# Kernel optimization log

Hardware: AMD Instinct MI355X
Metric: run time of the kernel (lower is better)

The kernel has to match this reference:

```python
import jax, jax.numpy as jnp
import numpy as np

D_MODEL = 64

def setup_inputs() -> dict:
    key = jax.random.key(0)
    kq, kk, kv = jax.random.split(key, 3)
    B, S, D = 8, 4096, D_MODEL
    q = jax.random.normal(kq, (B, S, D), dtype=jnp.float32)
    k = jax.random.normal(kk, (B, S, D), dtype=jnp.float32)
    v = jax.random.normal(kv, (B, S, D), dtype=jnp.float32)
    return {"q": q, "k": k, "v": v}

def reference(q, k, v):
    # scores: [B, S, S], scaled by 1/sqrt(d_model)
    scale = 1.0 / jnp.sqrt(jnp.asarray(D_MODEL, dtype=jnp.float32))
    scores = jnp.einsum("bqd,bkd->bqk", q, k) * scale
    attn = jax.nn.softmax(scores, axis=-1)
    return jnp.einsum("bqk,bkd->bqd", attn, v)
```

## Files before the change

kernel.cpp:

```cpp
#include <hip/hip_runtime.h>
#include <hip/hip_bf16.h>

#define NB 8
#define NS 4096
#define ND 64
#define NROW (NB * NS)
#define NTILE (NS / 64)

typedef short v4s __attribute__((ext_vector_type(4)));
typedef short v8s __attribute__((ext_vector_type(8)));
typedef float v4f __attribute__((ext_vector_type(4)));

static __device__ __forceinline__ v4s pk4(float a, float b, float c, float d) {
    union { __hip_bfloat162 h[2]; v4s v; } u;
    float2 p0; p0.x = a; p0.y = b;
    float2 p1; p1.x = c; p1.y = d;
    u.h[0] = __float22bfloat162_rn(p0);
    u.h[1] = __float22bfloat162_rn(p1);
    return u.v;
}
static __device__ __forceinline__ v8s pk8(v4f x0, v4f x1) {
    union { v4s q[2]; v8s v; } u;
    u.q[0] = pk4(x0[0], x0[1], x0[2], x0[3]);
    u.q[1] = pk4(x1[0], x1[1], x1[2], x1[3]);
    return u.v;
}
static __device__ __forceinline__ float b2f(short s) {
    return __uint_as_float(((unsigned)(unsigned short)s) << 16);
}

__device__ __forceinline__ void gl16(const void* g, void* s) {
    __builtin_amdgcn_global_load_lds(
        (const __attribute__((address_space(1))) void*)g,
        (__attribute__((address_space(3))) void*)s, 16, 0, 0);
}

__global__ __launch_bounds__(256) void prep_frag(const float* __restrict__ K,
        const float* __restrict__ V, short* __restrict__ Kf,
        short* __restrict__ Vf) {
    __shared__ short TK[64][72];
    __shared__ short TV[64][72];
    const int bt = blockIdx.x;
    const int b  = bt >> 6;
    const int s0 = (bt & 63) * 64;
    const int i  = threadIdx.x;
    #pragma unroll
    for (int it = 0; it < 4; ++it) {
        int n2 = it * 256 + i;
        int r = n2 >> 4, c4 = (n2 & 15) * 4;
        const size_t src = ((size_t)b * NS + s0 + r) * ND + c4;
        v4f xk = *(const v4f*)(K + src);
        v4f xv = *(const v4f*)(V + src);
        *(v4s*)&TK[r][c4] = pk4(xk[0], xk[1], xk[2], xk[3]);
        *(v4s*)&TV[r][c4] = pk4(xv[0], xv[1], xv[2], xv[3]);
    }
    __syncthreads();
    const size_t ob = (size_t)bt * 4096;
    #pragma unroll
    for (int it = 0; it < 2; ++it) {
        int gi = it * 256 + i;
        int lane = gi & 63, h = lane >> 4, lc = lane & 15;
        {
            int g = gi >> 7, c = (gi >> 6) & 1;
            v8s kk = *(const v8s*)&TK[16 * g + lc][32 * c + 8 * h];
            *(v8s*)&Kf[ob + (size_t)gi * 8] = kk;
        }
        {
            int c2 = gi >> 8, g = (gi >> 6) & 3;
            v8s vv;
            #pragma unroll
            for (int j = 0; j < 4; ++j) {
                vv[j]     = TV[32 * c2 + 4 * h + j][16 * g + lc];
                vv[4 + j] = TV[32 * c2 + 16 + 4 * h + j][16 * g + lc];
            }
            *(v8s*)&Vf[ob + (size_t)gi * 8] = vv;
        }
    }
}

template <int SPLIT>
__global__ __launch_bounds__(256, 4) void fa_main(
        const float* __restrict__ Q, const short* __restrict__ Kf,
        const short* __restrict__ Vf, float* __restrict__ O,
        short* __restrict__ Opart, float2* __restrict__ stats) {
    __shared__ short Ksh[2][4096];
    __shared__ short Vsh[2][4096];

    const int t    = threadIdx.x;
    const int lane = t & 63;
    const int w    = t >> 6;
    const int lc   = lane & 15;
    const int h    = lane >> 4;

    const int bid  = blockIdx.x;
    const int b    = bid & 7;
    const int rest = bid >> 3;
    const int sp   = rest % SPLIT;
    const int qblk = rest / SPLIT;
    const int q0   = qblk * 128 + w * 32;

    const int TPS = NTILE / SPLIT;
    const int kt0 = sp * TPS;

    const float SCL = 0.125f * 1.4426950408889634f;

    v8s qf[2][2];
    #pragma unroll
    for (int u = 0; u < 2; ++u) {
        const float* qrow = Q + ((size_t)b * NS + q0 + 16 * u + lc) * ND + 8 * h;
        #pragma unroll
        for (int c = 0; c < 2; ++c) {
            v4f x0 = *(const v4f*)(qrow + 32 * c);
            v4f x1 = *(const v4f*)(qrow + 32 * c + 4);
            qf[u][c] = pk8(x0 * SCL, x1 * SCL);
        }
    }

    v4f o[2][4];
    #pragma unroll
    for (int u = 0; u < 2; ++u)
        #pragma unroll
        for (int g = 0; g < 4; ++g) o[u][g] = (v4f){0.f, 0.f, 0.f, 0.f};
    float lsum[2] = {0.f, 0.f};

    const short* kfb = Kf + ((size_t)(b * NTILE + kt0)) * 4096 + t * 8;
    const short* vfb = Vf + ((size_t)(b * NTILE + kt0)) * 4096 + t * 8;
    auto stage = [&](int i, int buf) {
        const short* kb = kfb + (size_t)i * 4096;
        const short* vb = vfb + (size_t)i * 4096;
        short* kd = &Ksh[buf][t * 8];
        short* vd = &Vsh[buf][t * 8];
        gl16(kb,        kd);
        gl16(kb + 2048, kd + 2048);
        gl16(vb,        vd);
        gl16(vb + 2048, vd + 2048);
    };

    auto body = [&](int cur) {
        const short* kp = &Ksh[cur][lane * 8];
        const short* vp = &Vsh[cur][lane * 8];

        v4f a[2][4];
        #pragma unroll
        for (int g = 0; g < 4; ++g) {
            a[0][g] = (v4f){0.f, 0.f, 0.f, 0.f};
            a[1][g] = (v4f){0.f, 0.f, 0.f, 0.f};
            #pragma unroll
            for (int c = 0; c < 2; ++c) {
                v8s ka = *(const v8s*)(kp + (g * 2 + c) * 512);
                a[0][g] = __builtin_amdgcn_mfma_f32_16x16x32_bf16(ka, qf[0][c], a[0][g], 0, 0, 0);
                a[1][g] = __builtin_amdgcn_mfma_f32_16x16x32_bf16(ka, qf[1][c], a[1][g], 0, 0, 0);
            }
        }

        union PB { v4s q[2]; v8s v; } pb[2][2];
        #pragma unroll
        for (int u = 0; u < 2; ++u) {
            float rs = 0.f;
            #pragma unroll
            for (int g = 0; g < 4; ++g) {
                float e0 = __builtin_amdgcn_exp2f(a[u][g][0]);
                float e1 = __builtin_amdgcn_exp2f(a[u][g][1]);
                float e2 = __builtin_amdgcn_exp2f(a[u][g][2]);
                float e3 = __builtin_amdgcn_exp2f(a[u][g][3]);
                rs += (e0 + e1) + (e2 + e3);
                pb[u][g >> 1].q[g & 1] = pk4(e0, e1, e2, e3);
            }
            lsum[u] += rs;
        }

        #pragma unroll
        for (int c2 = 0; c2 < 2; ++c2) {
            #pragma unroll
            for (int g = 0; g < 4; ++g) {
                v8s va = *(const v8s*)(vp + (c2 * 4 + g) * 512);
                o[0][g] = __builtin_amdgcn_mfma_f32_16x16x32_bf16(va, pb[0][c2].v, o[0][g], 0, 0, 0);
                o[1][g] = __builtin_amdgcn_mfma_f32_16x16x32_bf16(va, pb[1][c2].v, o[1][g], 0, 0, 0);
            }
        }
    };

    stage(0, 0);
    int cur = 0;
    for (int i = 0; i < TPS; ++i) {
        __syncthreads();
        if (i + 1 < TPS) stage(i + 1, cur ^ 1);
        body(cur);
        cur ^= 1;
    }

    #pragma unroll
    for (int u = 0; u < 2; ++u) {
        float ls = lsum[u];
        ls += __shfl_xor(ls, 16);
        ls += __shfl_xor(ls, 32);
        const float inv = 1.0f / ls;
        const int q = q0 + 16 * u + lc;
        if constexpr (SPLIT == 1) {
            float* orow = O + ((size_t)b * NS + q) * ND;
            #pragma unroll
            for (int g = 0; g < 4; ++g) {
                v4f rr = o[u][g] * inv;
                *(v4f*)(orow + 16 * g + 4 * h) = rr;
            }
        } else {
            short* op = Opart + ((size_t)sp * NROW + (size_t)b * NS + q) * ND;
            #pragma unroll
            for (int g = 0; g < 4; ++g) {
                v4f rr = o[u][g] * inv;
                *(v4s*)(op + 16 * g + 4 * h) = pk4(rr[0], rr[1], rr[2], rr[3]);
            }
            if (h == 0) {
                float2 st; st.x = 0.f; st.y = ls;
                stats[(size_t)sp * NROW + (size_t)b * NS + q] = st;
            }
        }
    }
}

template <int SPLIT>
__global__ __launch_bounds__(256) void fa_combine(const short* __restrict__ Opart,
        const float2* __restrict__ stats, float* __restrict__ O) {
    const int idx = blockIdx.x * 256 + threadIdx.x;
    const int row = idx >> 3;
    const int d8  = (idx & 7) * 8;
    float2 st[SPLIT];
    float M = -INFINITY;
    #pragma unroll
    for (int s = 0; s < SPLIT; ++s) {
        st[s] = stats[(size_t)s * NROW + row];
        M = fmaxf(M, st[s].x);
    }
    float wt[SPLIT], wsum = 0.f;
    #pragma unroll
    for (int s = 0; s < SPLIT; ++s) {
        wt[s] = exp2f(st[s].x - M) * st[s].y;
        wsum += wt[s];
    }
    float acc[8] = {0.f, 0.f, 0.f, 0.f, 0.f, 0.f, 0.f, 0.f};
    #pragma unroll
    for (int s = 0; s < SPLIT; ++s) {
        v8s x = *(const v8s*)&Opart[((size_t)s * NROW + row) * ND + d8];
        #pragma unroll
        for (int j = 0; j < 8; ++j) acc[j] += wt[s] * b2f(x[j]);
    }
    const float inv = 1.0f / wsum;
    v4f r0, r1;
    #pragma unroll
    for (int j = 0; j < 4; ++j) { r0[j] = acc[j] * inv; r1[j] = acc[4 + j] * inv; }
    *(v4f*)&O[(size_t)row * ND + d8]     = r0;
    *(v4f*)&O[(size_t)row * ND + d8 + 4] = r1;
}

__global__ __launch_bounds__(256) void fa_fallback(
        const float* __restrict__ Q, const float* __restrict__ K,
        const float* __restrict__ V, float* __restrict__ O) {
    __shared__ short Ksh[64][72];
    __shared__ short Vsh[64][72];
    const int t = threadIdx.x;
    const int lane = t & 63;
    const int w = t >> 6;
    const int lc = lane & 15;
    const int h  = lane >> 4;
    const int b  = blockIdx.x & 7;
    const int q0 = (blockIdx.x >> 3) * 128 + w * 32;
    const float SCL = 0.125f * 1.4426950408889634f;
    v8s qf[2][2];
    #pragma unroll
    for (int u = 0; u < 2; ++u) {
        const float* qrow = Q + ((size_t)b * NS + q0 + 16 * u + lc) * ND + 8 * h;
        #pragma unroll
        for (int c = 0; c < 2; ++c) {
            v4f x0 = *(const v4f*)(qrow + 32 * c);
            v4f x1 = *(const v4f*)(qrow + 32 * c + 4);
            qf[u][c] = pk8(x0 * SCL, x1 * SCL);
        }
    }
    v4f o[2][4];
    #pragma unroll
    for (int u = 0; u < 2; ++u)
        #pragma unroll
        for (int g = 0; g < 4; ++g) o[u][g] = (v4f){0.f, 0.f, 0.f, 0.f};
    float m[2] = {-INFINITY, -INFINITY};
    float lsum[2] = {0.f, 0.f};
    for (int kt = 0; kt < NTILE; ++kt) {
        const int k0 = kt * 64;
        __syncthreads();
        #pragma unroll
        for (int i = 0; i < 4; ++i) {
            int n = i * 256 + t;
            int row = n >> 4, c4 = (n & 15) * 4;
            v4f x = *(const v4f*)(K + ((size_t)b * NS + k0 + row) * ND + c4);
            *(v4s*)&Ksh[row][c4] = pk4(x[0], x[1], x[2], x[3]);
        }
        const int sr = t >> 4, sc4 = t & 15;
        float xv[4][4];
        #pragma unroll
        for (int i = 0; i < 4; ++i) {
            v4f x = *(const v4f*)(V + ((size_t)b * NS + k0 + sr * 4 + i) * ND + sc4 * 4);
            xv[i][0] = x[0]; xv[i][1] = x[1]; xv[i][2] = x[2]; xv[i][3] = x[3];
        }
        #pragma unroll
        for (int j = 0; j < 4; ++j)
            *(v4s*)&Vsh[sc4 * 4 + j][sr * 4] = pk4(xv[0][j], xv[1][j], xv[2][j], xv[3][j]);
        __syncthreads();
        float p[2][4][4];
        #pragma unroll
        for (int g = 0; g < 4; ++g) {
            v4f a0 = (v4f){0.f, 0.f, 0.f, 0.f};
            v4f a1 = (v4f){0.f, 0.f, 0.f, 0.f};
            #pragma unroll
            for (int c = 0; c < 2; ++c) {
                v8s ka = *(const v8s*)&Ksh[16 * g + lc][32 * c + 8 * h];
                a0 = __builtin_amdgcn_mfma_f32_16x16x32_bf16(ka, qf[0][c], a0, 0, 0, 0);
                a1 = __builtin_amdgcn_mfma_f32_16x16x32_bf16(ka, qf[1][c], a1, 0, 0, 0);
            }
            #pragma unroll
            for (int r = 0; r < 4; ++r) { p[0][g][r] = a0[r]; p[1][g][r] = a1[r]; }
        }
        #pragma unroll
        for (int u = 0; u < 2; ++u) {
            float pm = p[u][0][0];
            #pragma unroll
            for (int g = 0; g < 4; ++g)
                #pragma unroll
                for (int r = 0; r < 4; ++r) pm = fmaxf(pm, p[u][g][r]);
            pm = fmaxf(pm, __shfl_xor(pm, 16));
            pm = fmaxf(pm, __shfl_xor(pm, 32));
            if (__any(pm > m[u] + 8.0f)) {
                float mn = fmaxf(m[u], pm);
                float al = __builtin_amdgcn_exp2f(m[u] - mn);
                #pragma unroll
                for (int g = 0; g < 4; ++g) o[u][g] = o[u][g] * al;
                lsum[u] *= al;
                m[u] = mn;
            }
            float rs = 0.f;
            #pragma unroll
            for (int g = 0; g < 4; ++g)
                #pragma unroll
                for (int r = 0; r < 4; ++r) {
                    p[u][g][r] = __builtin_amdgcn_exp2f(p[u][g][r] - m[u]);
                    rs += p[u][g][r];
                }
            lsum[u] += rs;
        }
        #pragma unroll
        for (int c2 = 0; c2 < 2; ++c2) {
            union { v4s q[2]; v8s v; } pb0, pb1;
            pb0.q[0] = pk4(p[0][2*c2][0],   p[0][2*c2][1],   p[0][2*c2][2],   p[0][2*c2][3]);
            pb0.q[1] = pk4(p[0][2*c2+1][0], p[0][2*c2+1][1], p[0][2*c2+1][2], p[0][2*c2+1][3]);
            pb1.q[0] = pk4(p[1][2*c2][0],   p[1][2*c2][1],   p[1][2*c2][2],   p[1][2*c2][3]);
            pb1.q[1] = pk4(p[1][2*c2+1][0], p[1][2*c2+1][1], p[1][2*c2+1][2], p[1][2*c2+1][3]);
            #pragma unroll
            for (int g = 0; g < 4; ++g) {
                union { v4s q[2]; v8s v; } va;
                va.q[0] = *(const v4s*)&Vsh[16 * g + lc][32 * c2 + 4 * h];
                va.q[1] = *(const v4s*)&Vsh[16 * g + lc][32 * c2 + 16 + 4 * h];
                o[0][g] = __builtin_amdgcn_mfma_f32_16x16x32_bf16(va.v, pb0.v, o[0][g], 0, 0, 0);
                o[1][g] = __builtin_amdgcn_mfma_f32_16x16x32_bf16(va.v, pb1.v, o[1][g], 0, 0, 0);
            }
        }
    }
    #pragma unroll
    for (int u = 0; u < 2; ++u) {
        float ls = lsum[u];
        ls += __shfl_xor(ls, 16);
        ls += __shfl_xor(ls, 32);
        float inv = 1.0f / ls;
        float* orow = O + ((size_t)b * NS + q0 + 16 * u + lc) * ND;
        #pragma unroll
        for (int g = 0; g < 4; ++g) {
            v4f rr = o[u][g] * inv;
            *(v4f*)(orow + 16 * g + 4 * h) = rr;
        }
    }
}

extern "C" void kernel_launch(void* const* d_in, const int* in_sizes, int n_in,
                              void* d_out, int out_size, void* d_ws, size_t ws_size,
                              hipStream_t stream) {
    const float* q = (const float*)d_in[0];
    const float* k = (const float*)d_in[1];
    const float* v = (const float*)d_in[2];
    float* out = (float*)d_out;

    const size_t tot   = (size_t)NB * NS * ND;
    const size_t kv    = 2 * tot * sizeof(short);
    const size_t per_s = tot * sizeof(short) + (size_t)NROW * sizeof(float2);
    const size_t need4 = kv + 4 * per_s;

    if (ws_size < kv) {
        hipLaunchKernelGGL(fa_fallback, dim3(NB * (NS / 128)), dim3(256), 0, stream,
                           q, k, v, out);
        return;
    }

    short* kf = (short*)d_ws;
    short* vf = kf + tot;
    short* opart = vf + tot;

    hipLaunchKernelGGL(prep_frag, dim3(NB * NTILE), dim3(256), 0, stream, k, v, kf, vf);

    if (ws_size >= need4) {
        float2* stats = (float2*)(opart + 4 * tot);
        hipLaunchKernelGGL(fa_main<4>, dim3(NB * 32 * 4), dim3(256), 0, stream,
                           q, kf, vf, out, opart, stats);
        hipLaunchKernelGGL(fa_combine<4>, dim3(NROW * 8 / 256), dim3(256), 0, stream,
                           opart, stats, out);
    } else {
        hipLaunchKernelGGL(fa_main<1>, dim3(NB * 32), dim3(256), 0, stream,
                           q, kf, vf, out, (short*)nullptr, (float2*)nullptr);
    }
}
```

Measured before the change: 56.12 us.

## Double query rows per warp, compute row sums via MFMA, add setprio

Measured after the change: 52.87 us. 5.8% less time.

```diff
diff --git a/kernel.cpp b/kernel.cpp
--- a/kernel.cpp
+++ b/kernel.cpp
@@ -79,7 +79,7 @@
 }
 
 template <int SPLIT>
-__global__ __launch_bounds__(256, 4) void fa_main(
+__global__ __launch_bounds__(256, 2) void fa_main(
         const float* __restrict__ Q, const short* __restrict__ Kf,
         const short* __restrict__ Vf, float* __restrict__ O,
         short* __restrict__ Opart, float2* __restrict__ stats) {
@@ -97,16 +97,19 @@
     const int rest = bid >> 3;
     const int sp   = rest % SPLIT;
     const int qblk = rest / SPLIT;
-    const int q0   = qblk * 128 + w * 32;
+    const int q0   = qblk * 256 + w * 64;
 
     const int TPS = NTILE / SPLIT;
     const int kt0 = sp * TPS;
 
     const float SCL = 0.125f * 1.4426950408889634f;
 
-    v8s qf[2][2];
-    #pragma unroll
-    for (int u = 0; u < 2; ++u) {
+    const short ONE = (short)0x3F80;
+    const v8s ones = {ONE, ONE, ONE, ONE, ONE, ONE, ONE, ONE};
+
+    v8s qf[4][2];
+    #pragma unroll
+    for (int u = 0; u < 4; ++u) {
         const float* qrow = Q + ((size_t)b * NS + q0 + 16 * u + lc) * ND + 8 * h;
         #pragma unroll
         for (int c = 0; c < 2; ++c) {
@@ -116,12 +119,14 @@
         }
     }
 
-    v4f o[2][4];
-    #pragma unroll
-    for (int u = 0; u < 2; ++u)
+    v4f o[4][4];
+    #pragma unroll
+    for (int u = 0; u < 4; ++u)
         #pragma unroll
         for (int g = 0; g < 4; ++g) o[u][g] = (v4f){0.f, 0.f, 0.f, 0.f};
-    float lsum[2] = {0.f, 0.f};
+    v4f ls[4];
+    #pragma unroll
+    for (int u = 0; u < 4; ++u) ls[u] = (v4f){0.f, 0.f, 0.f, 0.f};
 
     const short* kfb = Kf + ((size_t)(b * NTILE + kt0)) * 4096 + t * 8;
     const short* vfb = Vf + ((size_t)(b * NTILE + kt0)) * 4096 + t * 8;
@@ -140,44 +145,50 @@
         const short* kp = &Ksh[cur][lane * 8];
         const short* vp = &Vsh[cur][lane * 8];
 
-        v4f a[2][4];
+        v4f a[4][4];
+        __builtin_amdgcn_s_setprio(1);
         #pragma unroll
         for (int g = 0; g < 4; ++g) {
-            a[0][g] = (v4f){0.f, 0.f, 0.f, 0.f};
-            a[1][g] = (v4f){0.f, 0.f, 0.f, 0.f};
+            #pragma unroll
+            for (int u = 0; u < 4; ++u) a[u][g] = (v4f){0.f, 0.f, 0.f, 0.f};
             #pragma unroll
             for (int c = 0; c < 2; ++c) {
                 v8s ka = *(const v8s*)(kp + (g * 2 + c) * 512);
-                a[0][g] = __builtin_amdgcn_mfma_f32_16x16x32_bf16(ka, qf[0][c], a[0][g], 0, 0, 0);
-                a[1][g] = __builtin_amdgcn_mfma_f32_16x16x32_bf16(ka, qf[1][c], a[1][g], 0, 0, 0);
-            }
-        }
-
-        union PB { v4s q[2]; v8s v; } pb[2][2];
-        #pragma unroll
-        for (int u = 0; u < 2; ++u) {
-            float rs = 0.f;
+                #pragma unroll
+                for (int u = 0; u < 4; ++u)
+                    a[u][g] = __builtin_amdgcn_mfma_f32_16x16x32_bf16(ka, qf[u][c], a[u][g], 0, 0, 0);
+            }
+        }
+        __builtin_amdgcn_s_setprio(0);
+
+        union PB { v4s q[2]; v8s v; } pb[4][2];
+        #pragma unroll
+        for (int u = 0; u < 4; ++u) {
             #pragma unroll
             for (int g = 0; g < 4; ++g) {
                 float e0 = __builtin_amdgcn_exp2f(a[u][g][0]);
                 float e1 = __builtin_amdgcn_exp2f(a[u][g][1]);
                 float e2 = __builtin_amdgcn_exp2f(a[u][g][2]);
                 float e3 = __builtin_amdgcn_exp2f(a[u][g][3]);
-                rs += (e0 + e1) + (e2 + e3);
                 pb[u][g >> 1].q[g & 1] = pk4(e0, e1, e2, e3);
             }
-            lsum[u] += rs;
-        }
-
+        }
+
+        __builtin_amdgcn_s_setprio(1);
         #pragma unroll
         for (int c2 = 0; c2 < 2; ++c2) {
+            #pragma unroll
+            for (int u = 0; u < 4; ++u)
+                ls[u] = __builtin_amdgcn_mfma_f32_16x16x32_bf16(ones, pb[u][c2].v, ls[u], 0, 0, 0);
             #pragma unroll
             for (int g = 0; g < 4; ++g) {
                 v8s va = *(const v8s*)(vp + (c2 * 4 + g) * 512);
-                o[0][g] = __builtin_amdgcn_mfma_f32_16x16x32_bf16(va, pb[0][c2].v, o[0][g], 0, 0, 0);
-                o[1][g] = __builtin_amdgcn_mfma_f32_16x16x32_bf16(va, pb[1][c2].v, o[1][g], 0, 0, 0);
-            }
-        }
+                #pragma unroll
+                for (int u = 0; u < 4; ++u)
+                    o[u][g] = __builtin_amdgcn_mfma_f32_16x16x32_bf16(va, pb[u][c2].v, o[u][g], 0, 0, 0);
+            }
+        }
+        __builtin_amdgcn_s_setprio(0);
     };
 
     stage(0, 0);
@@ -190,11 +201,9 @@
     }
 
     #pragma unroll
-    for (int u = 0; u < 2; ++u) {
-        float ls = lsum[u];
-        ls += __shfl_xor(ls, 16);
-        ls += __shfl_xor(ls, 32);
-        const float inv = 1.0f / ls;
+    for (int u = 0; u < 4; ++u) {
+        const float lsv = ls[u][0];
+        const float inv = 1.0f / lsv;
         const int q = q0 + 16 * u + lc;
         if constexpr (SPLIT == 1) {
             float* orow = O + ((size_t)b * NS + q) * ND;
@@ -211,7 +220,7 @@
                 *(v4s*)(op + 16 * g + 4 * h) = pk4(rr[0], rr[1], rr[2], rr[3]);
             }
             if (h == 0) {
-                float2 st; st.x = 0.f; st.y = ls;
+                float2 st; st.x = 0.f; st.y = lsv;
                 stats[(size_t)sp * NROW + (size_t)b * NS + q] = st;
             }
         }
@@ -404,12 +413,12 @@
 
     if (ws_size >= need4) {
         float2* stats = (float2*)(opart + 4 * tot);
-        hipLaunchKernelGGL(fa_main<4>, dim3(NB * 32 * 4), dim3(256), 0, stream,
+        hipLaunchKernelGGL(fa_main<4>, dim3(NB * (NS / 256) * 4), dim3(256), 0, stream,
                            q, kf, vf, out, opart, stats);
         hipLaunchKernelGGL(fa_combine<4>, dim3(NROW * 8 / 256), dim3(256), 0, stream,
                            opart, stats, out);
     } else {
-        hipLaunchKernelGGL(fa_main<1>, dim3(NB * 32), dim3(256), 0, stream,
+        hipLaunchKernelGGL(fa_main<1>, dim3(NB * (NS / 256)), dim3(256), 0, stream,
                            q, kf, vf, out, (short*)nullptr, (float2*)nullptr);
     }
 }
```
